# Performance work log

Hardware: AMD Instinct MI355X
Metric: run time of the kernel (lower is better)

## Reference

```python
import jax, jax.numpy as jnp
import numpy as np

B, S, D, H, FF = 2, 2048, 512, 8, 2048
DK = D // H
EPS = 1e-3  # LayerNorm epsilon from the original module


def _layer_norm(x, gamma, beta):
    # biased variance over last dim, eps added inside sqrt (matches torch var_mean unbiased=False)
    mean = jnp.mean(x, axis=-1, keepdims=True)
    var = jnp.mean(jnp.square(x - mean), axis=-1, keepdims=True)
    return gamma * ((x - mean) / jnp.sqrt(var + EPS)) + beta


def setup_inputs() -> dict:
    key = jax.random.key(0)
    ks = jax.random.split(key, 16)
    sc = 0.02
    p = {
        'x': jax.random.normal(ks[0], (B, S, D), dtype=jnp.float32),
        'lengths': jax.random.randint(ks[1], (B,), 1, S + 1, dtype=jnp.int32),
        'Wq': jax.random.normal(ks[2], (D, D), dtype=jnp.float32) * sc,
        'bq': jnp.zeros((D,), dtype=jnp.float32),
        'Wk': jax.random.normal(ks[3], (D, D), dtype=jnp.float32) * sc,
        'bk': jnp.zeros((D,), dtype=jnp.float32),
        'Wv': jax.random.normal(ks[4], (D, D), dtype=jnp.float32) * sc,
        'bv': jnp.zeros((D,), dtype=jnp.float32),
        'Wo': jax.random.normal(ks[5], (D, D), dtype=jnp.float32) * sc,
        'bo': jnp.zeros((D,), dtype=jnp.float32),
        'W1': jax.random.normal(ks[6], (D, FF), dtype=jnp.float32) * sc,
        'b1': jnp.zeros((FF,), dtype=jnp.float32),
        'W2': jax.random.normal(ks[7], (FF, D), dtype=jnp.float32) * sc,
        'b2': jnp.zeros((D,), dtype=jnp.float32),
        'gamma1': jnp.ones((D,), dtype=jnp.float32),
        'beta1': jnp.zeros((D,), dtype=jnp.float32),
        'gamma2': jnp.ones((D,), dtype=jnp.float32),
        'beta2': jnp.zeros((D,), dtype=jnp.float32),
    }
    return p


def reference(x, lengths, Wq, bq, Wk, bk, Wv, bv, Wo, bo, W1, b1, W2, b2, gamma1, beta1, gamma2, beta2):
    neg_inf = jnp.float32(-jnp.inf)
    pos = jnp.arange(S)
    # pad mask: zero out padded token embeddings (create_pad_mask)
    pad = (pos[None, :] < lengths[:, None]).astype(x.dtype)  # (B, S)
    x = x * pad[:, :, None]

    # hand-rolled multi-head attention (NO 1/sqrt(d_k) scaling, matches original)
    q = (x @ Wq + bq).reshape(B, S, H, DK)
    k = (x @ Wk + bk).reshape(B, S, H, DK)
    v = (x @ Wv + bv).reshape(B, S, H, DK)
    scores = jnp.einsum('bshd,bqhd->bhsq', q, k)  # (B, H, S_query, S_key)

    # causal mask: key col j allowed iff j <= query row i
    causal = pos[None, :] <= pos[:, None]  # (S, S)
    # padding mask: key col j allowed iff j < lengths[b]
    keep = causal[None, None, :, :] & (pos[None, None, None, :] < lengths[:, None, None, None])
    scores = jnp.where(keep, scores, neg_inf)
    attn = jax.nn.softmax(scores, axis=-1)  # (B, H, S, S)

    # FAITHFUL to torch.einsum('bhss,bshd->bshd'): repeated 's' takes the DIAGONAL
    diag = jnp.einsum('bhss->bhs', attn)  # (B, H, S)
    weighted = diag.transpose(0, 2, 1)[:, :, :, None] * v  # (B, S, H, DK)
    attn_out = weighted.reshape(B, S, D) @ Wo + bo

    x = _layer_norm(x + attn_out, gamma1, beta1)
    ff = jax.nn.relu(x @ W1 + b1) @ W2 + b2  # dropout is identity in eval
    x = _layer_norm(x + ff, gamma2, beta2)
    return x
```

## Files before the change

### kernel.cpp

```cpp
#include <hip/hip_runtime.h>

#define B_   2
#define S_   2048
#define D_   512
#define H_   8
#define DK_  64
#define FF_  2048
#define EPS_ 1e-3f
#define QS_  1536

typedef __bf16 bf16;
typedef __bf16 bf16x4 __attribute__((ext_vector_type(4)));
typedef __bf16 bf16x8 __attribute__((ext_vector_type(8)));
typedef float  f32x4  __attribute__((ext_vector_type(4)));

struct Trans4Args {
  const float* w[4];
  bf16* thi[4];
  bf16* tlo[4];
  int rowOff[4];
};

__global__ __launch_bounds__(256) void transpose4_kernel(Trans4Args a) {
  __shared__ float tl[32][33];
  const int t = threadIdx.x;
  const int tx = t & 31, ty = t >> 5;
  const int n0 = blockIdx.x * 32, k0 = blockIdx.y * 32;
  const int wsel = blockIdx.z;
  const float* __restrict__ W = a.w[wsel];
#pragma unroll
  for (int r = 0; r < 32; r += 8)
    tl[r + ty][tx] = W[(size_t)(k0 + r + ty) * 512 + n0 + tx];
  __syncthreads();
  bf16* __restrict__ Thi = a.thi[wsel];
  bf16* __restrict__ Tlo = a.tlo[wsel];
  const int ro = a.rowOff[wsel];
#pragma unroll
  for (int r = 0; r < 32; r += 8) {
    const int n = r + ty;
    const float v = tl[tx][n];
    const bf16 h = (bf16)v;
    const size_t o = (size_t)(ro + n0 + n) * 512 + k0 + tx;
    Thi[o] = h;
    Tlo[o] = (bf16)(v - (float)h);
  }
}

__global__ __launch_bounds__(256) void transpose_split_kernel(
    const float* __restrict__ W, int K, int N,
    bf16* __restrict__ Thi, bf16* __restrict__ Tlo) {
  __shared__ float tl[32][33];
  const int t = threadIdx.x;
  const int tx = t & 31, ty = t >> 5;
  const int n0 = blockIdx.x * 32, k0 = blockIdx.y * 32;
#pragma unroll
  for (int r = 0; r < 32; r += 8)
    tl[r + ty][tx] = W[(size_t)(k0 + r + ty) * N + n0 + tx];
  __syncthreads();
#pragma unroll
  for (int r = 0; r < 32; r += 8) {
    const int n = r + ty;
    const float v = tl[tx][n];
    const bf16 h = (bf16)v;
    const size_t o = (size_t)(n0 + n) * K + k0 + tx;
    Thi[o] = h;
    Tlo[o] = (bf16)(v - (float)h);
  }
}

__global__ __launch_bounds__(256) void pack_bias_kernel(const float* __restrict__ bq,
                                                        const float* __restrict__ bk,
                                                        const float* __restrict__ bv,
                                                        float* __restrict__ out) {
  const int i = blockIdx.x * 256 + threadIdx.x;
  out[i] = (i < 512) ? bq[i] : (i < 1024) ? bk[i - 512] : bv[i - 1024];
}

__global__ __launch_bounds__(256) void mask_split_kernel(const float* __restrict__ x,
                                                         const int* __restrict__ lengths,
                                                         bf16* __restrict__ xhi,
                                                         bf16* __restrict__ xlo) {
  const int idx = blockIdx.x * 256 + threadIdx.x;
  const int d4 = D_ / 4;
  const int s = (idx / d4) & (S_ - 1);
  const int b = idx / (d4 * S_);
  float4 v = reinterpret_cast<const float4*>(x)[idx];
  if (s >= lengths[b]) { v.x = 0.f; v.y = 0.f; v.z = 0.f; v.w = 0.f; }
  const float vv[4] = {v.x, v.y, v.z, v.w};
  bf16x4 h, l;
#pragma unroll
  for (int c = 0; c < 4; ++c) {
    const bf16 hh = (bf16)vv[c];
    h[c] = hh;
    l[c] = (bf16)(vv[c] - (float)hh);
  }
  reinterpret_cast<bf16x4*>(xhi)[idx] = h;
  reinterpret_cast<bf16x4*>(xlo)[idx] = l;
}

enum { EPI_BIAS_RELU = 2, EPI_PART = 4, EPI_QKV = 5 };

template <int EPI, bool SPLIT>
__global__ __launch_bounds__(256) void gemm_kernel(
    const bf16* __restrict__ Ahi, const bf16* __restrict__ Alo,
    const bf16* __restrict__ Bhi, const bf16* __restrict__ Blo,
    const float* __restrict__ bias,
    float* __restrict__ C, float* __restrict__ C2,
    bf16* __restrict__ Chi, bf16* __restrict__ Clo,
    int K, int ldc, int nx, int mn, int ksplit) {
  __shared__ __align__(16) bf16 As[2][64][40];
  __shared__ __align__(16) bf16 Bs[2][64][40];
  const int t = threadIdx.x;

  const int nwg = gridDim.x;
  const int chunk = nwg >> 3;
  const int virt = (blockIdx.x & 7) * chunk + (blockIdx.x >> 3);
  const int s = virt / mn;
  const int v2 = virt - s * mn;
  const int m0 = (v2 / nx) * 64, n0 = (v2 % nx) * 64;
  const int kb = s * ksplit;

  const int ar = t >> 2, ak = (t & 3) * 8;
  const int lane = t & 63, wv = t >> 6;
  const int wm = (wv >> 1) * 32, wn = (wv & 1) * 32;
  const int fr = lane & 15, fg = lane >> 4;

  f32x4 acc[2][2] = {};

  const bf16* pAhi = Ahi + (size_t)(m0 + ar) * K + kb + ak;
  const bf16* pAlo = Alo + (size_t)(m0 + ar) * K + kb + ak;
  const bf16* pBhi = Bhi + (size_t)(n0 + ar) * K + kb + ak;
  const bf16* pBlo = Blo + (size_t)(n0 + ar) * K + kb + ak;

  for (int k0 = 0; k0 < ksplit; k0 += 32) {
    *reinterpret_cast<int4*>(&As[0][ar][ak]) = *reinterpret_cast<const int4*>(pAhi + k0);
    *reinterpret_cast<int4*>(&As[1][ar][ak]) = *reinterpret_cast<const int4*>(pAlo + k0);
    *reinterpret_cast<int4*>(&Bs[0][ar][ak]) = *reinterpret_cast<const int4*>(pBhi + k0);
    *reinterpret_cast<int4*>(&Bs[1][ar][ak]) = *reinterpret_cast<const int4*>(pBlo + k0);
    __syncthreads();

    bf16x8 ah[2], al[2], bh[2], bl[2];
#pragma unroll
    for (int m = 0; m < 2; ++m) {
      ah[m] = *reinterpret_cast<const bf16x8*>(&As[0][wm + m * 16 + fr][fg * 8]);
      al[m] = *reinterpret_cast<const bf16x8*>(&As[1][wm + m * 16 + fr][fg * 8]);
      bh[m] = *reinterpret_cast<const bf16x8*>(&Bs[0][wn + m * 16 + fr][fg * 8]);
      bl[m] = *reinterpret_cast<const bf16x8*>(&Bs[1][wn + m * 16 + fr][fg * 8]);
    }
#pragma unroll
    for (int m = 0; m < 2; ++m)
#pragma unroll
      for (int n = 0; n < 2; ++n) {
        acc[m][n] = __builtin_amdgcn_mfma_f32_16x16x32_bf16(bh[n], ah[m], acc[m][n], 0, 0, 0);
        acc[m][n] = __builtin_amdgcn_mfma_f32_16x16x32_bf16(bl[n], ah[m], acc[m][n], 0, 0, 0);
        acc[m][n] = __builtin_amdgcn_mfma_f32_16x16x32_bf16(bh[n], al[m], acc[m][n], 0, 0, 0);
      }
    __syncthreads();
  }

  float* __restrict__ Cw = (s == 0) ? C : C2;
#pragma unroll
  for (int m = 0; m < 2; ++m) {
    const int row = m0 + wm + m * 16 + fr;
#pragma unroll
    for (int n = 0; n < 2; ++n) {
      const int col = n0 + wn + n * 16 + fg * 4;
      f32x4 v = acc[m][n];
      if constexpr (EPI != EPI_PART) {
        const f32x4 b4 = *reinterpret_cast<const f32x4*>(bias + col);
#pragma unroll
        for (int c = 0; c < 4; ++c) v[c] += b4[c];
      }
      if constexpr (EPI == EPI_BIAS_RELU) {
#pragma unroll
        for (int c = 0; c < 4; ++c) v[c] = fmaxf(v[c], 0.f);
      }
      if constexpr (EPI == EPI_QKV) {
        if (col < 1024) {
          bf16x4 h, l;
#pragma unroll
          for (int c = 0; c < 4; ++c) {
            const bf16 hh = (bf16)v[c];
            h[c] = hh;
            l[c] = (bf16)(v[c] - (float)hh);
          }
          *reinterpret_cast<bf16x4*>(&Chi[(size_t)row * 1024 + col]) = h;
          *reinterpret_cast<bf16x4*>(&Clo[(size_t)row * 1024 + col]) = l;
        } else {
          *reinterpret_cast<f32x4*>(&C[(size_t)row * D_ + col - 1024]) = v;
        }
      } else if constexpr (SPLIT) {
        bf16x4 h, l;
#pragma unroll
        for (int c = 0; c < 4; ++c) {
          const bf16 hh = (bf16)v[c];
          h[c] = hh;
          l[c] = (bf16)(v[c] - (float)hh);
        }
        *reinterpret_cast<bf16x4*>(&Chi[(size_t)row * ldc + col]) = h;
        *reinterpret_cast<bf16x4*>(&Clo[(size_t)row * ldc + col]) = l;
      } else {
        *reinterpret_cast<f32x4*>(&Cw[(size_t)row * ldc + col]) = v;
      }
    }
  }
}

__global__ __launch_bounds__(256) void attn_part_kernel(
    const bf16* __restrict__ qk_hi, const bf16* __restrict__ qk_lo,
    const int* __restrict__ lengths,
    float* __restrict__ pm, float* __restrict__ pl, float* __restrict__ pd) {
  __shared__ __align__(16) bf16 Qh[64][72], Ql[64][72];
  __shared__ __align__(16) bf16 Kh[64][72], Kl[64][72];
  const int t = threadIdx.x;
  const int lane = t & 63, wv = t >> 6;
  const int fr = lane & 15, fg = lane >> 4;
  const int bh = blockIdx.y;
  const int bb = bh >> 3, h = bh & 7;

  const int p = blockIdx.x;
  int a = (int)sqrtf((float)p);
  while ((a + 1) * (a + 1) <= p) ++a;
  while (a * a > p) --a;
  int ib, jc;
  if (p >= a * a + a) { ib = 2 * a;     jc = p - (a * a + a); }
  else                { ib = 2 * a - 1; jc = p - a * a; }

  const int i0 = ib * 64;
  const int len = lengths[bb];
  if (i0 >= len || jc * 128 >= len) return;

  const int sr = t >> 2, sc0 = (t & 3) * 16;
  {
    const size_t gb = (size_t)(bb * S_ + i0 + sr) * 1024 + h * DK_ + sc0;
    *reinterpret_cast<int4*>(&Qh[sr][sc0])     = *reinterpret_cast<const int4*>(qk_hi + gb);
    *reinterpret_cast<int4*>(&Qh[sr][sc0 + 8]) = *reinterpret_cast<const int4*>(qk_hi + gb + 8);
    *reinterpret_cast<int4*>(&Ql[sr][sc0])     = *reinterpret_cast<const int4*>(qk_lo + gb);
    *reinterpret_cast<int4*>(&Ql[sr][sc0 + 8]) = *reinterpret_cast<const int4*>(qk_lo + gb + 8);
  }

  float m_r[4], l_r[4], d_r[4];
#pragma unroll
  for (int r = 0; r < 4; ++r) { m_r[r] = -1e30f; l_r[r] = 0.f; d_r[r] = 0.f; }

  const int jlim = min(i0 + 63, len - 1);
  for (int jt = 0; jt < 2; ++jt) {
    const int j0 = jc * 128 + jt * 64;
    if (j0 > jlim) break;
    {
      const size_t gb = (size_t)(bb * S_ + j0 + sr) * 1024 + 512 + h * DK_ + sc0;
      *reinterpret_cast<int4*>(&Kh[sr][sc0])     = *reinterpret_cast<const int4*>(qk_hi + gb);
      *reinterpret_cast<int4*>(&Kh[sr][sc0 + 8]) = *reinterpret_cast<const int4*>(qk_hi + gb + 8);
      *reinterpret_cast<int4*>(&Kl[sr][sc0])     = *reinterpret_cast<const int4*>(qk_lo + gb);
      *reinterpret_cast<int4*>(&Kl[sr][sc0 + 8]) = *reinterpret_cast<const int4*>(qk_lo + gb + 8);
    }
    __syncthreads();

    f32x4 sc[4] = {};
#pragma unroll
    for (int kk = 0; kk < 2; ++kk) {
      const bf16x8 qh = *reinterpret_cast<const bf16x8*>(&Qh[wv * 16 + fr][kk * 32 + fg * 8]);
      const bf16x8 ql = *reinterpret_cast<const bf16x8*>(&Ql[wv * 16 + fr][kk * 32 + fg * 8]);
#pragma unroll
      for (int jf = 0; jf < 4; ++jf) {
        const bf16x8 kh = *reinterpret_cast<const bf16x8*>(&Kh[jf * 16 + fr][kk * 32 + fg * 8]);
        const bf16x8 kl = *reinterpret_cast<const bf16x8*>(&Kl[jf * 16 + fr][kk * 32 + fg * 8]);
        sc[jf] = __builtin_amdgcn_mfma_f32_16x16x32_bf16(qh, kh, sc[jf], 0, 0, 0);
        sc[jf] = __builtin_amdgcn_mfma_f32_16x16x32_bf16(qh, kl, sc[jf], 0, 0, 0);
        sc[jf] = __builtin_amdgcn_mfma_f32_16x16x32_bf16(ql, kh, sc[jf], 0, 0, 0);
      }
    }

#pragma unroll
    for (int r = 0; r < 4; ++r) {
      const int ig = i0 + wv * 16 + fg * 4 + r;
      float s4[4];
      float mx = -1e30f;
#pragma unroll
      for (int jf = 0; jf < 4; ++jf) {
        const int j = j0 + jf * 16 + fr;
        float v = sc[jf][r];
        if (j > ig || j >= len) v = -1e30f;
        s4[jf] = v;
        mx = fmaxf(mx, v);
      }
#pragma unroll
      for (int off = 1; off < 16; off <<= 1) mx = fmaxf(mx, __shfl_xor(mx, off));
      const float mnew = fmaxf(m_r[r], mx);
      float ps = 0.f, pdg = 0.f;
#pragma unroll
      for (int jf = 0; jf < 4; ++jf) {
        const float e = __expf(s4[jf] - mnew);
        ps += e;
        if (j0 + jf * 16 + fr == ig) pdg = e;
      }
#pragma unroll
      for (int off = 1; off < 16; off <<= 1) {
        ps += __shfl_xor(ps, off);
        pdg += __shfl_xor(pdg, off);
      }
      const float scale = __expf(m_r[r] - mnew);
      l_r[r] = l_r[r] * scale + ps;
      d_r[r] = d_r[r] * scale + pdg;
      m_r[r] = mnew;
    }
    __syncthreads();
  }

  if (fr == 0) {
    const size_t base = ((size_t)(bh * 32 + ib) * 16 + jc) * 64;
#pragma unroll
    for (int r = 0; r < 4; ++r) {
      const int row = wv * 16 + fg * 4 + r;
      const float mm = m_r[r];
      const bool ok = mm > -1e29f;
      pm[base + row] = mm;
      pl[base + row] = ok ? l_r[r] : 0.f;
      pd[base + row] = ok ? d_r[r] : 0.f;
    }
  }
}

__global__ __launch_bounds__(256) void attn_merge_kernel(
    const float* __restrict__ vsrc, const int* __restrict__ lengths,
    const float* __restrict__ pm, const float* __restrict__ pl,
    const float* __restrict__ pd, bf16* __restrict__ whi, bf16* __restrict__ wlo) {
  __shared__ float msh[4][64], lsh[4][64], dsh[4][64];
  __shared__ float dgs[64];
  const int t = threadIdx.x;
  const int ib = blockIdx.x, bh = blockIdx.y;
  const int bb = bh >> 3, h = bh & 7;
  const int i0 = ib * 64;
  const int len = lengths[bb];

  const int r = t & 63, g = t >> 6;
  float m = -1e30f, l = 0.f, d = 0.f;
  if (i0 < len) {
    const int jcmax = min((i0 + 63) >> 7, (len - 1) >> 7);
    const size_t base = ((size_t)(bh * 32 + ib) * 16) * 64 + r;
    for (int jc = g; jc <= jcmax; jc += 4) {
      const size_t idx = base + (size_t)jc * 64;
      const float m2 = pm[idx], l2 = pl[idx], d2 = pd[idx];
      const float mn = fmaxf(m, m2);
      const float e1 = __expf(m - mn), e2 = __expf(m2 - mn);
      l = l * e1 + l2 * e2;
      d = d * e1 + d2 * e2;
      m = mn;
    }
  }
  msh[g][r] = m; lsh[g][r] = l; dsh[g][r] = d;
  __syncthreads();
  if (t < 64) {
    float M = msh[0][t], L = lsh[0][t], Dv = dsh[0][t];
#pragma unroll
    for (int gg = 1; gg < 4; ++gg) {
      const float m2 = msh[gg][t], l2 = lsh[gg][t], d2 = dsh[gg][t];
      const float mn = fmaxf(M, m2);
      const float e1 = __expf(M - mn), e2 = __expf(m2 - mn);
      L = L * e1 + l2 * e2;
      Dv = Dv * e1 + d2 * e2;
      M = mn;
    }
    dgs[t] = (i0 + t < len) ? Dv / L : 0.f;
  }
  __syncthreads();

  const int rr = t >> 2, q = t & 3;
  const float dg = dgs[rr];
  const size_t obase = (size_t)(bb * S_ + i0 + rr) * D_ + h * DK_;
#pragma unroll
  for (int kk = 0; kk < 4; ++kk) {
    const int col = q * 4 + kk * 16;
    const float4 v4 = *reinterpret_cast<const float4*>(vsrc + obase + col);
    const float vv[4] = {dg * v4.x, dg * v4.y, dg * v4.z, dg * v4.w};
    bf16x4 hh, ll;
#pragma unroll
    for (int c = 0; c < 4; ++c) {
      const bf16 x = (bf16)vv[c];
      hh[c] = x;
      ll[c] = (bf16)(vv[c] - (float)x);
    }
    *reinterpret_cast<bf16x4*>(&whi[obase + col]) = hh;
    *reinterpret_cast<bf16x4*>(&wlo[obase + col]) = ll;
  }
}

__global__ __launch_bounds__(256) void ln1_fused_kernel(
    const float* __restrict__ P0, const float* __restrict__ P1,
    const float* __restrict__ x, const int* __restrict__ lengths,
    const float* __restrict__ bo,
    const float* __restrict__ gamma, const float* __restrict__ beta,
    bf16* __restrict__ Yhi, bf16* __restrict__ Ylo) {
  const int row = blockIdx.x;
  const int t = threadIdx.x;
  const int lenb = lengths[row >> 11];
  const bool valid = (row & (S_ - 1)) < lenb;
  const size_t ro = (size_t)row * D_ + t * 2;
  const float2 p0 = *reinterpret_cast<const float2*>(P0 + ro);
  const float2 p1 = *reinterpret_cast<const float2*>(P1 + ro);
  const float2 xv = *reinterpret_cast<const float2*>(x + ro);
  const float2 bv = *reinterpret_cast<const float2*>(bo + t * 2);
  float hx = p0.x + p1.x + bv.x + (valid ? xv.x : 0.f);
  float hy = p0.y + p1.y + bv.y + (valid ? xv.y : 0.f);

  float s = hx + hy, s2 = hx * hx + hy * hy;
#pragma unroll
  for (int off = 1; off < 64; off <<= 1) {
    s += __shfl_xor(s, off);
    s2 += __shfl_xor(s2, off);
  }
  __shared__ float red[8];
  const int w = t >> 6;
  if ((t & 63) == 0) { red[w] = s; red[4 + w] = s2; }
  __syncthreads();
  const float ts  = red[0] + red[1] + red[2] + red[3];
  const float ts2 = red[4] + red[5] + red[6] + red[7];
  const float mean = ts * (1.f / D_);
  const float var  = ts2 * (1.f / D_) - mean * mean;
  const float inv  = 1.f / sqrtf(var + EPS_);
  const float2 g  = *reinterpret_cast<const float2*>(gamma + t * 2);
  const float2 bt = *reinterpret_cast<const float2*>(beta + t * 2);
  const float ox = g.x * ((hx - mean) * inv) + bt.x;
  const float oy = g.y * ((hy - mean) * inv) + bt.y;
  const bf16 ohx = (bf16)ox, ohy = (bf16)oy;
  Yhi[ro] = ohx;  Yhi[ro + 1] = ohy;
  Ylo[ro] = (bf16)(ox - (float)ohx);
  Ylo[ro + 1] = (bf16)(oy - (float)ohy);
}

__global__ __launch_bounds__(256) void ln2_fused_kernel(
    const float* __restrict__ Q0, const float* __restrict__ Q1,
    const bf16* __restrict__ Yhi, const bf16* __restrict__ Ylo,
    const float* __restrict__ b2,
    const float* __restrict__ gamma, const float* __restrict__ beta,
    float* __restrict__ out) {
  const int row = blockIdx.x;
  const int t = threadIdx.x;
  const size_t ro = (size_t)row * D_ + t * 2;
  const float2 q0 = *reinterpret_cast<const float2*>(Q0 + ro);
  const float2 q1 = *reinterpret_cast<const float2*>(Q1 + ro);
  const float2 bv = *reinterpret_cast<const float2*>(b2 + t * 2);
  const float y1x = (float)Yhi[ro] + (float)Ylo[ro];
  const float y1y = (float)Yhi[ro + 1] + (float)Ylo[ro + 1];
  float hx = q0.x + q1.x + bv.x + y1x;
  float hy = q0.y + q1.y + bv.y + y1y;

  float s = hx + hy, s2 = hx * hx + hy * hy;
#pragma unroll
  for (int off = 1; off < 64; off <<= 1) {
    s += __shfl_xor(s, off);
    s2 += __shfl_xor(s2, off);
  }
  __shared__ float red[8];
  const int w = t >> 6;
  if ((t & 63) == 0) { red[w] = s; red[4 + w] = s2; }
  __syncthreads();
  const float ts  = red[0] + red[1] + red[2] + red[3];
  const float ts2 = red[4] + red[5] + red[6] + red[7];
  const float mean = ts * (1.f / D_);
  const float var  = ts2 * (1.f / D_) - mean * mean;
  const float inv  = 1.f / sqrtf(var + EPS_);
  const float2 g  = *reinterpret_cast<const float2*>(gamma + t * 2);
  const float2 bt = *reinterpret_cast<const float2*>(beta + t * 2);
  float2 o;
  o.x = g.x * ((hx - mean) * inv) + bt.x;
  o.y = g.y * ((hy - mean) * inv) + bt.y;
  *reinterpret_cast<float2*>(out + ro) = o;
}

extern "C" void kernel_launch(void* const* d_in, const int* in_sizes, int n_in,
                              void* d_out, int out_size, void* d_ws, size_t ws_size,
                              hipStream_t stream) {
  const float* x       = (const float*)d_in[0];
  const int*   lengths = (const int*)d_in[1];
  const float* Wq = (const float*)d_in[2];
  const float* bq = (const float*)d_in[3];
  const float* Wk = (const float*)d_in[4];
  const float* bk = (const float*)d_in[5];
  const float* Wv = (const float*)d_in[6];
  const float* bv = (const float*)d_in[7];
  const float* Wo = (const float*)d_in[8];
  const float* bo = (const float*)d_in[9];
  const float* W1 = (const float*)d_in[10];
  const float* b1 = (const float*)d_in[11];
  const float* W2 = (const float*)d_in[12];
  const float* b2 = (const float*)d_in[13];
  const float* gamma1 = (const float*)d_in[14];
  const float* beta1  = (const float*)d_in[15];
  const float* gamma2 = (const float*)d_in[16];
  const float* beta2  = (const float*)d_in[17];
  float* out = (float*)d_out;

  char* ws = (char*)d_ws;
  bf16*  qkvT_hi = (bf16*)(ws + 0);
  bf16*  qkvT_lo = (bf16*)(ws + 1572864);
  bf16*  WoT_hi  = (bf16*)(ws + 3145728);
  bf16*  WoT_lo  = (bf16*)(ws + 3670016);
  bf16*  W1T_hi  = (bf16*)(ws + 4194304);
  bf16*  W1T_lo  = (bf16*)(ws + 6291456);
  bf16*  W2T_hi  = (bf16*)(ws + 8388608);
  bf16*  W2T_lo  = (bf16*)(ws + 10485760);
  float* bqkv    = (float*)(ws + 12582912);
  bf16*  qk_hi   = (bf16*)(ws + 12589056);
  bf16*  qk_lo   = (bf16*)(ws + 20977664);
  float* v_f32   = (float*)(ws + 29366272);
  float* P0      = (float*)(ws + 12589056);
  float* P1      = (float*)(ws + 20977664);
  float* part_m  = (float*)(ws + 37754880);
  float* part_l  = (float*)(ws + 39852032);
  float* part_d  = (float*)(ws + 41949184);
  bf16*  ff1_hi  = (bf16*)(ws + 12589056);
  bf16*  ff1_lo  = (bf16*)(ws + 29366272);
  bf16*  xm_hi   = (bf16*)(ws + 46143488);
  bf16*  xm_lo   = (bf16*)(ws + 50337792);
  bf16*  y1_hi   = (bf16*)(ws + 46143488);
  bf16*  y1_lo   = (bf16*)(ws + 50337792);
  bf16*  wgt_hi  = (bf16*)(ws + 54532096);
  bf16*  wgt_lo  = (bf16*)(ws + 58726400);
  float* Q0      = (float*)(ws + 54532096);
  float* Q1      = (float*)(ws + 0);

  const dim3 blk(256);
  const int M = B_ * S_;

  Trans4Args ta;
  ta.w[0] = Wq; ta.w[1] = Wk; ta.w[2] = Wv; ta.w[3] = Wo;
  ta.thi[0] = qkvT_hi; ta.thi[1] = qkvT_hi; ta.thi[2] = qkvT_hi; ta.thi[3] = WoT_hi;
  ta.tlo[0] = qkvT_lo; ta.tlo[1] = qkvT_lo; ta.tlo[2] = qkvT_lo; ta.tlo[3] = WoT_lo;
  ta.rowOff[0] = 0; ta.rowOff[1] = 512; ta.rowOff[2] = 1024; ta.rowOff[3] = 0;
  transpose4_kernel<<<dim3(16, 16, 4), blk, 0, stream>>>(ta);
  transpose_split_kernel<<<dim3(64, 16), blk, 0, stream>>>(W1, 512, 2048, W1T_hi, W1T_lo);
  transpose_split_kernel<<<dim3(16, 64), blk, 0, stream>>>(W2, 2048, 512, W2T_hi, W2T_lo);
  pack_bias_kernel<<<dim3(6), blk, 0, stream>>>(bq, bk, bv, bqkv);

  mask_split_kernel<<<dim3((M * D_ / 4) / 256), blk, 0, stream>>>(x, lengths, xm_hi, xm_lo);

  gemm_kernel<EPI_QKV, false><<<dim3(1536), blk, 0, stream>>>(
      xm_hi, xm_lo, qkvT_hi, qkvT_lo, bqkv,
      v_f32, nullptr, qk_hi, qk_lo, 512, QS_, 24, 1536, 512);

  attn_part_kernel<<<dim3(272, 16), blk, 0, stream>>>(qk_hi, qk_lo, lengths,
                                                      part_m, part_l, part_d);
  attn_merge_kernel<<<dim3(32, 16), blk, 0, stream>>>(v_f32, lengths, part_m, part_l, part_d,
                                                      wgt_hi, wgt_lo);

  gemm_kernel<EPI_PART, false><<<dim3(1024), blk, 0, stream>>>(
      wgt_hi, wgt_lo, WoT_hi, WoT_lo, nullptr,
      P0, P1, nullptr, nullptr, 512, D_, 8, 512, 256);

  ln1_fused_kernel<<<dim3(M), blk, 0, stream>>>(P0, P1, x, lengths, bo,
                                                gamma1, beta1, y1_hi, y1_lo);

  gemm_kernel<EPI_BIAS_RELU, true><<<dim3(2048), blk, 0, stream>>>(
      y1_hi, y1_lo, W1T_hi, W1T_lo, b1,
      nullptr, nullptr, ff1_hi, ff1_lo, 512, FF_, 32, 2048, 512);

  gemm_kernel<EPI_PART, false><<<dim3(1024), blk, 0, stream>>>(
      ff1_hi, ff1_lo, W2T_hi, W2T_lo, nullptr,
      Q0, Q1, nullptr, nullptr, FF_, D_, 8, 512, 1024);

  ln2_fused_kernel<<<dim3(M), blk, 0, stream>>>(Q0, Q1, y1_hi, y1_lo, b2,
                                                gamma2, beta2, out);
}
```

Before: 286.2 us.

## Enlarge GEMM tiles to 128xBN and load via direct global-to-LDS with XOR swizzle

The split-bf16 GEMM now uses 128-row tiles with a templated N tile (128 or 64), so each wave holds 4xNR accumulators and reuses each staged fragment more. Tiles are loaded with global_load_lds 16-byte transfers into unpadded shared arrays, using an XOR swizzle on the 8-element chunks to avoid bank conflicts. Grid sizes are cut to match the larger tiles. This aims to reduce global and LDS traffic per FLOP and register staging, at the cost of fewer workgroups (weaker occupancy and load balance) and more register pressure.

```diff
diff --git a/kernel.cpp b/kernel.cpp
--- a/kernel.cpp
+++ b/kernel.cpp
@@ -13,6 +13,12 @@
 typedef __bf16 bf16x4 __attribute__((ext_vector_type(4)));
 typedef __bf16 bf16x8 __attribute__((ext_vector_type(8)));
 typedef float  f32x4  __attribute__((ext_vector_type(4)));
+
+__device__ __forceinline__ void gload16(const bf16* g, bf16* l) {
+  __builtin_amdgcn_global_load_lds(
+      (__attribute__((address_space(1))) void*)g,
+      (__attribute__((address_space(3))) void*)l, 16, 0, 0);
+}
 
 struct Trans4Args {
   const float* w[4];
@@ -100,7 +106,7 @@
 
 enum { EPI_BIAS_RELU = 2, EPI_PART = 4, EPI_QKV = 5 };
 
-template <int EPI, bool SPLIT>
+template <int EPI, bool SPLIT, int BN>
 __global__ __launch_bounds__(256) void gemm_kernel(
     const bf16* __restrict__ Ahi, const bf16* __restrict__ Alo,
     const bf16* __restrict__ Bhi, const bf16* __restrict__ Blo,
@@ -108,8 +114,9 @@
     float* __restrict__ C, float* __restrict__ C2,
     bf16* __restrict__ Chi, bf16* __restrict__ Clo,
     int K, int ldc, int nx, int mn, int ksplit) {
-  __shared__ __align__(16) bf16 As[2][64][40];
-  __shared__ __align__(16) bf16 Bs[2][64][40];
+  constexpr int NR = BN / 32;
+  __shared__ __align__(16) bf16 As[2][128][32];
+  __shared__ __align__(16) bf16 Bs[2][BN][32];
   const int t = threadIdx.x;
 
   const int nwg = gridDim.x;
@@ -117,40 +124,67 @@
   const int virt = (blockIdx.x & 7) * chunk + (blockIdx.x >> 3);
   const int s = virt / mn;
   const int v2 = virt - s * mn;
-  const int m0 = (v2 / nx) * 64, n0 = (v2 % nx) * 64;
+  const int m0 = (v2 / nx) * 128, n0 = (v2 % nx) * BN;
   const int kb = s * ksplit;
 
-  const int ar = t >> 2, ak = (t & 3) * 8;
   const int lane = t & 63, wv = t >> 6;
-  const int wm = (wv >> 1) * 32, wn = (wv & 1) * 32;
   const int fr = lane & 15, fg = lane >> 4;
-
-  f32x4 acc[2][2] = {};
-
-  const bf16* pAhi = Ahi + (size_t)(m0 + ar) * K + kb + ak;
-  const bf16* pAlo = Alo + (size_t)(m0 + ar) * K + kb + ak;
-  const bf16* pBhi = Bhi + (size_t)(n0 + ar) * K + kb + ak;
-  const bf16* pBlo = Blo + (size_t)(n0 + ar) * K + kb + ak;
+  const int wm = (wv >> 1) * 64, wn = (wv & 1) * (BN / 2);
+  const int sr = lane >> 2, sslot = lane & 3;
+
+  f32x4 acc[4][NR] = {};
+
+  const bf16* gAh = Ahi + (size_t)m0 * K + kb;
+  const bf16* gAl = Alo + (size_t)m0 * K + kb;
+  const bf16* gBh = Bhi + (size_t)n0 * K + kb;
+  const bf16* gBl = Blo + (size_t)n0 * K + kb;
 
   for (int k0 = 0; k0 < ksplit; k0 += 32) {
-    *reinterpret_cast<int4*>(&As[0][ar][ak]) = *reinterpret_cast<const int4*>(pAhi + k0);
-    *reinterpret_cast<int4*>(&As[1][ar][ak]) = *reinterpret_cast<const int4*>(pAlo + k0);
-    *reinterpret_cast<int4*>(&Bs[0][ar][ak]) = *reinterpret_cast<const int4*>(pBhi + k0);
-    *reinterpret_cast<int4*>(&Bs[1][ar][ak]) = *reinterpret_cast<const int4*>(pBlo + k0);
+#pragma unroll
+    for (int q = 0; q < 2; ++q) {
+      const int r = wv * 32 + q * 16 + sr;
+      const int ch = sslot ^ ((r >> 1) & 3);
+      const size_t go = (size_t)r * K + k0 + ch * 8;
+      gload16(gAh + go, &As[0][wv * 32 + q * 16][0]);
+      gload16(gAl + go, &As[1][wv * 32 + q * 16][0]);
+    }
+    if constexpr (BN == 128) {
+#pragma unroll
+      for (int q = 0; q < 2; ++q) {
+        const int r = wv * 32 + q * 16 + sr;
+        const int ch = sslot ^ ((r >> 1) & 3);
+        const size_t go = (size_t)r * K + k0 + ch * 8;
+        gload16(gBh + go, &Bs[0][wv * 32 + q * 16][0]);
+        gload16(gBl + go, &Bs[1][wv * 32 + q * 16][0]);
+      }
+    } else {
+      const int r = wv * 16 + sr;
+      const int ch = sslot ^ ((r >> 1) & 3);
+      const size_t go = (size_t)r * K + k0 + ch * 8;
+      gload16(gBh + go, &Bs[0][wv * 16][0]);
+      gload16(gBl + go, &Bs[1][wv * 16][0]);
+    }
     __syncthreads();
 
-    bf16x8 ah[2], al[2], bh[2], bl[2];
-#pragma unroll
-    for (int m = 0; m < 2; ++m) {
-      ah[m] = *reinterpret_cast<const bf16x8*>(&As[0][wm + m * 16 + fr][fg * 8]);
-      al[m] = *reinterpret_cast<const bf16x8*>(&As[1][wm + m * 16 + fr][fg * 8]);
-      bh[m] = *reinterpret_cast<const bf16x8*>(&Bs[0][wn + m * 16 + fr][fg * 8]);
-      bl[m] = *reinterpret_cast<const bf16x8*>(&Bs[1][wn + m * 16 + fr][fg * 8]);
-    }
-#pragma unroll
-    for (int m = 0; m < 2; ++m)
-#pragma unroll
-      for (int n = 0; n < 2; ++n) {
+    bf16x8 ah[4], al[4], bh[NR], bl[NR];
+#pragma unroll
+    for (int m = 0; m < 4; ++m) {
+      const int r = wm + m * 16 + fr;
+      const int ch = fg ^ ((r >> 1) & 3);
+      ah[m] = *reinterpret_cast<const bf16x8*>(&As[0][r][ch * 8]);
+      al[m] = *reinterpret_cast<const bf16x8*>(&As[1][r][ch * 8]);
+    }
+#pragma unroll
+    for (int n = 0; n < NR; ++n) {
+      const int r = wn + n * 16 + fr;
+      const int ch = fg ^ ((r >> 1) & 3);
+      bh[n] = *reinterpret_cast<const bf16x8*>(&Bs[0][r][ch * 8]);
+      bl[n] = *reinterpret_cast<const bf16x8*>(&Bs[1][r][ch * 8]);
+    }
+#pragma unroll
+    for (int m = 0; m < 4; ++m)
+#pragma unroll
+      for (int n = 0; n < NR; ++n) {
         acc[m][n] = __builtin_amdgcn_mfma_f32_16x16x32_bf16(bh[n], ah[m], acc[m][n], 0, 0, 0);
         acc[m][n] = __builtin_amdgcn_mfma_f32_16x16x32_bf16(bl[n], ah[m], acc[m][n], 0, 0, 0);
         acc[m][n] = __builtin_amdgcn_mfma_f32_16x16x32_bf16(bh[n], al[m], acc[m][n], 0, 0, 0);
@@ -160,10 +194,10 @@
 
   float* __restrict__ Cw = (s == 0) ? C : C2;
 #pragma unroll
-  for (int m = 0; m < 2; ++m) {
+  for (int m = 0; m < 4; ++m) {
     const int row = m0 + wm + m * 16 + fr;
 #pragma unroll
-    for (int n = 0; n < 2; ++n) {
+    for (int n = 0; n < NR; ++n) {
       const int col = n0 + wn + n * 16 + fg * 4;
       f32x4 v = acc[m][n];
       if constexpr (EPI != EPI_PART) {
@@ -535,29 +569,29 @@
 
   mask_split_kernel<<<dim3((M * D_ / 4) / 256), blk, 0, stream>>>(x, lengths, xm_hi, xm_lo);
 
-  gemm_kernel<EPI_QKV, false><<<dim3(1536), blk, 0, stream>>>(
+  gemm_kernel<EPI_QKV, false, 128><<<dim3(384), blk, 0, stream>>>(
       xm_hi, xm_lo, qkvT_hi, qkvT_lo, bqkv,
-      v_f32, nullptr, qk_hi, qk_lo, 512, QS_, 24, 1536, 512);
+      v_f32, nullptr, qk_hi, qk_lo, 512, QS_, 12, 384, 512);
 
   attn_part_kernel<<<dim3(272, 16), blk, 0, stream>>>(qk_hi, qk_lo, lengths,
                                                       part_m, part_l, part_d);
   attn_merge_kernel<<<dim3(32, 16), blk, 0, stream>>>(v_f32, lengths, part_m, part_l, part_d,
                                                       wgt_hi, wgt_lo);
 
-  gemm_kernel<EPI_PART, false><<<dim3(1024), blk, 0, stream>>>(
+  gemm_kernel<EPI_PART, false, 64><<<dim3(512), blk, 0, stream>>>(
       wgt_hi, wgt_lo, WoT_hi, WoT_lo, nullptr,
-      P0, P1, nullptr, nullptr, 512, D_, 8, 512, 256);
+      P0, P1, nullptr, nullptr, 512, D_, 8, 256, 256);
 
   ln1_fused_kernel<<<dim3(M), blk, 0, stream>>>(P0, P1, x, lengths, bo,
                                                 gamma1, beta1, y1_hi, y1_lo);
 
-  gemm_kernel<EPI_BIAS_RELU, true><<<dim3(2048), blk, 0, stream>>>(
+  gemm_kernel<EPI_BIAS_RELU, true, 128><<<dim3(512), blk, 0, stream>>>(
       y1_hi, y1_lo, W1T_hi, W1T_lo, b1,
-      nullptr, nullptr, ff1_hi, ff1_lo, 512, FF_, 32, 2048, 512);
-
-  gemm_kernel<EPI_PART, false><<<dim3(1024), blk, 0, stream>>>(
+      nullptr, nullptr, ff1_hi, ff1_lo, 512, FF_, 16, 512, 512);
+
+  gemm_kernel<EPI_PART, false, 64><<<dim3(512), blk, 0, stream>>>(
       ff1_hi, ff1_lo, W2T_hi, W2T_lo, nullptr,
-      Q0, Q1, nullptr, nullptr, FF_, D_, 8, 512, 1024);
+      Q0, Q1, nullptr, nullptr, FF_, D_, 8, 256, 1024);
 
   ln2_fused_kernel<<<dim3(M), blk, 0, stream>>>(Q0, Q1, y1_hi, y1_lo, b2,
                                                 gamma2, beta2, out);
```

New measurement: 266.2 us. -7.0%, faster.
